# Performance work log

Hardware: AMD Instinct MI355X
Metric: run time of the kernel (lower is better)

## Reference

```python
import jax, jax.numpy as jnp
import numpy as np

SEQ_LEN = 48
OUT_DIM = 3
EMB_DIM = 32
HID_DIM = 96
BATCH = 131072


def setup_inputs() -> dict:
    key = jax.random.key(0)
    ks = jax.random.split(key, 12)
    s_emb = 1.0 / np.sqrt(OUT_DIM)
    s_gru = 1.0 / np.sqrt(HID_DIM)
    s_out = 1.0 / np.sqrt(HID_DIM)
    u = lambda k, shp, s: jax.random.uniform(k, shp, jnp.float32, -s, s)
    return {
        "last_pos_rel": jax.random.normal(ks[0], (BATCH, OUT_DIM), jnp.float32),
        "past_encoded": jax.random.normal(ks[1], (1, BATCH, HID_DIM // 2), jnp.float32),
        "future_encoded": jax.random.normal(ks[2], (1, BATCH, HID_DIM // 2), jnp.float32),
        "W_emb": u(ks[3], (EMB_DIM, OUT_DIM), s_emb),
        "b_emb": u(ks[4], (EMB_DIM,), s_emb),
        "W_ih": u(ks[5], (3 * HID_DIM, EMB_DIM), s_gru),
        "W_hh": u(ks[6], (3 * HID_DIM, HID_DIM), s_gru),
        "b_ih": u(ks[7], (3 * HID_DIM,), s_gru),
        "b_hh": u(ks[8], (3 * HID_DIM,), s_gru),
        "W_out": u(ks[9], (OUT_DIM, HID_DIM), s_out),
        "b_out": u(ks[10], (OUT_DIM,), s_out),
    }


def reference(last_pos_rel, past_encoded, future_encoded, W_emb, b_emb,
              W_ih, W_hh, b_ih, b_hh, W_out, b_out):
    # initial hidden state: concat of the two 48-dim encodings -> (B, 96)
    h0 = jnp.concatenate([past_encoded, future_encoded], axis=2)[0]
    # initial decoder input: spatial embedding of last relative position
    x0 = last_pos_rel @ W_emb.T + b_emb  # (B, EMB)

    def step(carry, _):
        h, x = carry
        gx = x @ W_ih.T + b_ih   # (B, 3H)
        gh = h @ W_hh.T + b_hh   # (B, 3H)
        gxr, gxz, gxn = jnp.split(gx, 3, axis=-1)
        ghr, ghz, ghn = jnp.split(gh, 3, axis=-1)
        r = jax.nn.sigmoid(gxr + ghr)
        z = jax.nn.sigmoid(gxz + ghz)
        n = jnp.tanh(gxn + r * ghn)
        h_new = (1.0 - z) * n + z * h
        rel_pos = h_new @ W_out.T + b_out       # (B, 3)
        x_new = rel_pos @ W_emb.T + b_emb       # (B, EMB)
        return (h_new, x_new), rel_pos

    _, pred_traj = jax.lax.scan(step, (h0, x0), None, length=SEQ_LEN)
    return pred_traj  # (SEQ_LEN, B, 3)
```

## Files before the change

### kernel.cpp

```cpp
#include <hip/hip_runtime.h>
#include <hip/hip_bf16.h>
#include <type_traits>

#define SEQ_LEN 48
#define HID     96
#define NB      131072
#define MROWS   304
#define ABYTES  (MROWS*HID*2)
#define COEF_OFF_F (ABYTES/4)
#define COEF_FLOATS (96*16)
#define BOUT_OFF_F (COEF_OFF_F + COEF_FLOATS)
#define LDS_U4  ((ABYTES + COEF_FLOATS*4)/16)

typedef __attribute__((ext_vector_type(4))) float f32x4;
typedef __attribute__((ext_vector_type(8))) __bf16 bf16x8;
typedef unsigned int uint;
typedef unsigned short ushort;

__device__ __forceinline__ float sigm(float x) {
    return __builtin_amdgcn_rcpf(1.f + __expf(-x));
}
__device__ __forceinline__ float tanh_(float y) {
    return 1.f - 2.f * __builtin_amdgcn_rcpf(__expf(2.f * y) + 1.f);
}
__device__ __forceinline__ uint packbf(float a, float b) {
    ushort lo = __builtin_bit_cast(ushort, __float2bfloat16(a));
    ushort hi = __builtin_bit_cast(ushort, __float2bfloat16(b));
    return (uint)lo | ((uint)hi << 16);
}

__global__ void fold_k(const float* __restrict__ W_emb, const float* __restrict__ b_emb,
                       const float* __restrict__ W_ih,  const float* __restrict__ W_hh,
                       const float* __restrict__ b_ih,  const float* __restrict__ b_hh,
                       const float* __restrict__ W_out, const float* __restrict__ b_out,
                       void* wsv)
{
    ushort* A  = (ushort*)wsv;
    float*  CF = (float*)wsv + COEF_OFF_F;
    float*  BO = (float*)wsv + BOUT_OFF_F;
    int g = blockIdx.x * 64 + threadIdx.x;
    if (g < 3) BO[g] = b_out[g];

    auto wxe_row = [&](int gg, float* w, float& bx) {
        w[0] = w[1] = w[2] = 0.f; bx = b_ih[gg];
        for (int e = 0; e < 32; e++) {
            float wi = W_ih[gg * 32 + e];
            w[0] += wi * W_emb[e * 3 + 0];
            w[1] += wi * W_emb[e * 3 + 1];
            w[2] += wi * W_emb[e * 3 + 2];
            bx   += wi * b_emb[e];
        }
    };

    if (g < MROWS) {
        float w[3] = {0.f, 0.f, 0.f}, bx = 0.f;
        if (g < 192) wxe_row(g, w, bx);
        for (int k = 0; k < HID; k++) {
            float val;
            if      (g < 192) val = W_hh[g * HID + k] + w[0]*W_out[0*HID+k] + w[1]*W_out[1*HID+k] + w[2]*W_out[2*HID+k];
            else if (g < 288) val = W_hh[g * HID + k];
            else if (g < 291) val = W_out[(g - 288) * HID + k];
            else              val = 0.f;
            int t = g >> 4, c = k >> 5, l = (g & 15) | (((k >> 3) & 3) << 4), i = k & 7;
            A[((t * 3 + c) * 64 + l) * 8 + i] = __builtin_bit_cast(ushort, __float2bfloat16(val));
        }
    }
    if (g < 96) {
        int j = g;
        float wn[3], bxn; wxe_row(192 + j, wn, bxn);
        float wr[3], bxr; wxe_row(j,        wr, bxr);
        float wz[3], bxz; wxe_row(96 + j,   wz, bxz);
        float quads[4][4] = {
            { wn[0], wn[1], wn[2], bxn },
            { b_hh[192 + j],
              bxr + b_hh[j]      + wr[0]*b_out[0] + wr[1]*b_out[1] + wr[2]*b_out[2],
              bxz + b_hh[96 + j] + wz[0]*b_out[0] + wz[1]*b_out[1] + wz[2]*b_out[2],
              0.f },
            { wr[0], wr[1], wr[2], wz[0] },
            { wz[1], wz[2], 0.f, 0.f }
        };
        int qj = (j >> 2) & 3;
        float* row = CF + j * 16;
        for (int L = 0; L < 4; ++L) {
            int p = (L + qj) & 3;
            row[p * 4 + 0] = quads[L][0];
            row[p * 4 + 1] = quads[L][1];
            row[p * 4 + 2] = quads[L][2];
            row[p * 4 + 3] = quads[L][3];
        }
    }
}

__global__ __launch_bounds__(256, 2)
void gru_mfma(const float* __restrict__ last_pos, const float* __restrict__ past,
              const float* __restrict__ fut, const void* __restrict__ wsv,
              float* __restrict__ out)
{
    __shared__ uint4 sb[LDS_U4];
    const int tid = threadIdx.x;
    const uint4* gsrc = (const uint4*)wsv;
    #pragma unroll
    for (int it = 0; it < 16; ++it) { int idx = tid + it * 256; if (idx < LDS_U4) sb[idx] = gsrc[idx]; }
    __syncthreads();

    const float* CF  = (const float*)sb + COEF_OFF_F;
    const float* BOg = (const float*)wsv + BOUT_OFF_F;
    const float bo[3] = {BOg[0], BOg[1], BOg[2]};

    const int lane = tid & 63;
    const int wid  = tid >> 6;
    const int b    = lane & 15;
    const int q    = lane >> 4;
    const int row0 = blockIdx.x * 64 + wid * 16 + b;

    uint hpk[6][2];
    #pragma unroll
    for (int t = 0; t < 6; ++t) {
        const float* src = (t < 3) ? (past + (size_t)row0 * 48 + t * 16 + q * 4)
                                   : (fut  + (size_t)row0 * 48 + (t - 3) * 16 + q * 4);
        f32x4 v = *(const f32x4*)src;
        hpk[t][0] = packbf(v[0], v[1]);
        hpk[t][1] = packbf(v[2], v[3]);
    }

    const int idxA = 4 * (b | ((((q << 1) + 0) & 3) << 4));
    const int idxB = 4 * (b | ((((q << 1) + 1) & 3) << 4));
    uint4 bfu[3];
    auto do_exchange = [&]() {
        #pragma unroll
        for (int c = 0; c < 3; ++c)
            #pragma unroll
            for (int dd = 0; dd < 4; ++dd) {
                int idx = (dd < 2) ? idxA : idxB;
                int va = __builtin_amdgcn_ds_bpermute(idx, (int)hpk[2 * c][dd & 1]);
                int vb = __builtin_amdgcn_ds_bpermute(idx, (int)hpk[2 * c + 1][dd & 1]);
                bfu[c][dd] = (uint)((lane < 32) ? va : vb);
            }
    };
    do_exchange();

    float pc[3];
    pc[0] = last_pos[(size_t)row0 * 3 + 0];
    pc[1] = last_pos[(size_t)row0 * 3 + 1];
    pc[2] = last_pos[(size_t)row0 * 3 + 2];

    const f32x4 zero4 = {0.f, 0.f, 0.f, 0.f};
    const int p0r = (0 + q) & 3, p1r = (1 + q) & 3, p2r = (2 + q) & 3, p3r = (3 + q) & 3;

    auto tile18 = [&]() -> f32x4 {
        f32x4 a18;
        #pragma unroll
        for (int c = 0; c < 3; ++c) {
            bf16x8 a = __builtin_bit_cast(bf16x8, sb[(18 * 3 + c) * 64 + lane]);
            bf16x8 bb = __builtin_bit_cast(bf16x8, bfu[c]);
            a18 = __builtin_amdgcn_mfma_f32_16x16x32_bf16(a, bb, (c == 0) ? zero4 : a18, 0, 0, 0);
        }
        return a18;
    };

    auto do_groups = [&](auto FIRST_c, const float* d0) {
        constexpr bool FIRST = decltype(FIRST_c)::value;
        #pragma unroll
        for (int t = 0; t < 6; ++t) {
            f32x4 aR, aZ, aN;
            #pragma unroll
            for (int c = 0; c < 3; ++c) {
                bf16x8 fr = __builtin_bit_cast(bf16x8, sb[((t)      * 3 + c) * 64 + lane]);
                bf16x8 fz = __builtin_bit_cast(bf16x8, sb[((6 + t)  * 3 + c) * 64 + lane]);
                bf16x8 fn = __builtin_bit_cast(bf16x8, sb[((12 + t) * 3 + c) * 64 + lane]);
                bf16x8 bb = __builtin_bit_cast(bf16x8, bfu[c]);
                aR = __builtin_amdgcn_mfma_f32_16x16x32_bf16(fr, bb, (c == 0) ? zero4 : aR, 0, 0, 0);
                aZ = __builtin_amdgcn_mfma_f32_16x16x32_bf16(fz, bb, (c == 0) ? zero4 : aZ, 0, 0, 0);
                aN = __builtin_amdgcn_mfma_f32_16x16x32_bf16(fn, bb, (c == 0) ? zero4 : aN, 0, 0, 0);
            }
            const float* cbase = CF + (16 * t + 4 * q) * 16;
            uint np0 = 0, np1 = 0;
            #pragma unroll
            for (int r = 0; r < 4; ++r) {
                f32x4 ca = *(const f32x4*)(cbase + 16 * r + 4 * p0r);
                f32x4 cb = *(const f32x4*)(cbase + 16 * r + 4 * p1r);
                float sr  = aR[r] + cb[1];
                float sz  = aZ[r] + cb[2];
                float ghn = aN[r] + cb[0];
                float gxn = ca[3] + pc[0]*ca[0] + pc[1]*ca[1] + pc[2]*ca[2];
                if constexpr (FIRST) {
                    f32x4 c2 = *(const f32x4*)(cbase + 16 * r + 4 * p2r);
                    f32x4 c3 = *(const f32x4*)(cbase + 16 * r + 4 * p3r);
                    sr += d0[0]*c2[0] + d0[1]*c2[1] + d0[2]*c2[2];
                    sz += d0[0]*c2[3] + d0[1]*c3[0] + d0[2]*c3[1];
                }
                float rg = sigm(sr);
                float zg = sigm(sz);
                float ng = tanh_(gxn + rg * ghn);
                uint pk = hpk[t][r >> 1];
                float hold = __builtin_bit_cast(float, (r & 1) ? (pk & 0xffff0000u) : (pk << 16));
                float hv = ng + zg * (hold - ng);
                ushort hb = __builtin_bit_cast(ushort, __float2bfloat16(hv));
                if      (r == 0) np0 = hb;
                else if (r == 1) np0 |= (uint)hb << 16;
                else if (r == 2) np1 = hb;
                else             np1 |= (uint)hb << 16;
            }
            hpk[t][0] = np0;
            hpk[t][1] = np1;
            __builtin_amdgcn_sched_barrier(0);
        }
    };

    {
        f32x4 a18 = tile18();
        float d0[3];
        #pragma unroll
        for (int o = 0; o < 3; ++o) {
            float po = a18[o] + bo[o];
            float pb = __builtin_bit_cast(float,
                        __builtin_amdgcn_ds_bpermute(4 * b, __builtin_bit_cast(int, po)));
            d0[o] = pc[o] - pb;
        }
        __builtin_amdgcn_sched_barrier(0);
        do_groups(std::integral_constant<bool, true>{}, d0);
        do_exchange();
    }

    #pragma unroll 1
    for (int s = 1; s < SEQ_LEN; ++s) {
        f32x4 a18 = tile18();
        #pragma unroll
        for (int o = 0; o < 3; ++o) {
            float po = a18[o] + bo[o];
            float pb = __builtin_bit_cast(float,
                        __builtin_amdgcn_ds_bpermute(4 * b, __builtin_bit_cast(int, po)));
            if (q == 0) out[((size_t)(s - 1) * NB + row0) * 3 + o] = po;
            pc[o] = pb;
        }
        __builtin_amdgcn_sched_barrier(0);
        do_groups(std::integral_constant<bool, false>{}, nullptr);
        do_exchange();
    }

    {
        f32x4 f18 = tile18();
        if (q == 0) {
            #pragma unroll
            for (int o = 0; o < 3; ++o)
                out[((size_t)47 * NB + row0) * 3 + o] = f18[o] + bo[o];
        }
    }
}

extern "C" void kernel_launch(void* const* d_in, const int* in_sizes, int n_in,
                              void* d_out, int out_size, void* d_ws, size_t ws_size,
                              hipStream_t stream)
{
    const float* last_pos = (const float*)d_in[0];
    const float* past     = (const float*)d_in[1];
    const float* fut      = (const float*)d_in[2];
    const float* W_emb    = (const float*)d_in[3];
    const float* b_emb    = (const float*)d_in[4];
    const float* W_ih     = (const float*)d_in[5];
    const float* W_hh     = (const float*)d_in[6];
    const float* b_ih     = (const float*)d_in[7];
    const float* b_hh     = (const float*)d_in[8];
    const float* W_out    = (const float*)d_in[9];
    const float* b_out    = (const float*)d_in[10];
    float* out = (float*)d_out;

    hipLaunchKernelGGL(fold_k, dim3(5), dim3(64), 0, stream,
                       W_emb, b_emb, W_ih, W_hh, b_ih, b_hh, W_out, b_out, d_ws);
    hipLaunchKernelGGL(gru_mfma, dim3(NB / 64), dim3(256), 0, stream,
                       last_pos, past, fut, d_ws, out);
}
```

Before: 842.7 us.

## Fold log2(e) into GRU weights and use 512-thread blocks

The preprocessing kernel now pre-scales the r/z gate weights and biases by log2(e) and the n-gate terms by 2*log2(e). The recurrent kernel can then call the hardware exp2 directly, dropping one multiply per transcendental in the inner gate math. Separately, blocks grow to 512 threads covering 128 rows, with launch bounds asking for 4 blocks per CU. That tightens the per-thread register budget, which may force spills, and the roughly 64 KB of LDS per block likely caps real residency below the requested 4 blocks.

```diff
diff --git a/kernel.cpp b/kernel.cpp
--- a/kernel.cpp
+++ b/kernel.cpp
@@ -17,11 +17,11 @@
 typedef unsigned int uint;
 typedef unsigned short ushort;
 
-__device__ __forceinline__ float sigm(float x) {
-    return __builtin_amdgcn_rcpf(1.f + __expf(-x));
-}
-__device__ __forceinline__ float tanh_(float y) {
-    return 1.f - 2.f * __builtin_amdgcn_rcpf(__expf(2.f * y) + 1.f);
+__device__ __forceinline__ float sigm2(float xp) {
+    return __builtin_amdgcn_rcpf(1.f + __builtin_amdgcn_exp2f(-xp));
+}
+__device__ __forceinline__ float tanh2(float yp) {
+    return 1.f - 2.f * __builtin_amdgcn_rcpf(__builtin_amdgcn_exp2f(yp) + 1.f);
 }
 __device__ __forceinline__ uint packbf(float a, float b) {
     ushort lo = __builtin_bit_cast(ushort, __float2bfloat16(a));
@@ -35,6 +35,8 @@
                        const float* __restrict__ W_out, const float* __restrict__ b_out,
                        void* wsv)
 {
+    const float L2E  = 1.44269504088896340736f;
+    const float L2E2 = 2.f * L2E;
     ushort* A  = (ushort*)wsv;
     float*  CF = (float*)wsv + COEF_OFF_F;
     float*  BO = (float*)wsv + BOUT_OFF_F;
@@ -57,8 +59,8 @@
         if (g < 192) wxe_row(g, w, bx);
         for (int k = 0; k < HID; k++) {
             float val;
-            if      (g < 192) val = W_hh[g * HID + k] + w[0]*W_out[0*HID+k] + w[1]*W_out[1*HID+k] + w[2]*W_out[2*HID+k];
-            else if (g < 288) val = W_hh[g * HID + k];
+            if      (g < 192) val = (W_hh[g * HID + k] + w[0]*W_out[0*HID+k] + w[1]*W_out[1*HID+k] + w[2]*W_out[2*HID+k]) * L2E;
+            else if (g < 288) val = W_hh[g * HID + k] * L2E2;
             else if (g < 291) val = W_out[(g - 288) * HID + k];
             else              val = 0.f;
             int t = g >> 4, c = k >> 5, l = (g & 15) | (((k >> 3) & 3) << 4), i = k & 7;
@@ -71,13 +73,13 @@
         float wr[3], bxr; wxe_row(j,        wr, bxr);
         float wz[3], bxz; wxe_row(96 + j,   wz, bxz);
         float quads[4][4] = {
-            { wn[0], wn[1], wn[2], bxn },
-            { b_hh[192 + j],
-              bxr + b_hh[j]      + wr[0]*b_out[0] + wr[1]*b_out[1] + wr[2]*b_out[2],
-              bxz + b_hh[96 + j] + wz[0]*b_out[0] + wz[1]*b_out[1] + wz[2]*b_out[2],
+            { wn[0]*L2E2, wn[1]*L2E2, wn[2]*L2E2, bxn*L2E2 },
+            { b_hh[192 + j]*L2E2,
+              (bxr + b_hh[j]      + wr[0]*b_out[0] + wr[1]*b_out[1] + wr[2]*b_out[2]) * L2E,
+              (bxz + b_hh[96 + j] + wz[0]*b_out[0] + wz[1]*b_out[1] + wz[2]*b_out[2]) * L2E,
               0.f },
-            { wr[0], wr[1], wr[2], wz[0] },
-            { wz[1], wz[2], 0.f, 0.f }
+            { wr[0]*L2E, wr[1]*L2E, wr[2]*L2E, wz[0]*L2E },
+            { wz[1]*L2E, wz[2]*L2E, 0.f, 0.f }
         };
         int qj = (j >> 2) & 3;
         float* row = CF + j * 16;
@@ -91,7 +93,7 @@
     }
 }
 
-__global__ __launch_bounds__(256, 2)
+__global__ __launch_bounds__(512, 4)
 void gru_mfma(const float* __restrict__ last_pos, const float* __restrict__ past,
               const float* __restrict__ fut, const void* __restrict__ wsv,
               float* __restrict__ out)
@@ -100,7 +102,7 @@
     const int tid = threadIdx.x;
     const uint4* gsrc = (const uint4*)wsv;
     #pragma unroll
-    for (int it = 0; it < 16; ++it) { int idx = tid + it * 256; if (idx < LDS_U4) sb[idx] = gsrc[idx]; }
+    for (int it = 0; it < 8; ++it) { int idx = tid + it * 512; if (idx < LDS_U4) sb[idx] = gsrc[idx]; }
     __syncthreads();
 
     const float* CF  = (const float*)sb + COEF_OFF_F;
@@ -111,7 +113,7 @@
     const int wid  = tid >> 6;
     const int b    = lane & 15;
     const int q    = lane >> 4;
-    const int row0 = blockIdx.x * 64 + wid * 16 + b;
+    const int row0 = blockIdx.x * 128 + wid * 16 + b;
 
     uint hpk[6][2];
     #pragma unroll
@@ -189,9 +191,9 @@
                     sr += d0[0]*c2[0] + d0[1]*c2[1] + d0[2]*c2[2];
                     sz += d0[0]*c2[3] + d0[1]*c3[0] + d0[2]*c3[1];
                 }
-                float rg = sigm(sr);
-                float zg = sigm(sz);
-                float ng = tanh_(gxn + rg * ghn);
+                float rg = sigm2(sr);
+                float zg = sigm2(sz);
+                float ng = tanh2(gxn + rg * ghn);
                 uint pk = hpk[t][r >> 1];
                 float hold = __builtin_bit_cast(float, (r & 1) ? (pk & 0xffff0000u) : (pk << 16));
                 float hv = ng + zg * (hold - ng);
@@ -267,6 +269,6 @@
 
     hipLaunchKernelGGL(fold_k, dim3(5), dim3(64), 0, stream,
                        W_emb, b_emb, W_ih, W_hh, b_ih, b_hh, W_out, b_out, d_ws);
-    hipLaunchKernelGGL(gru_mfma, dim3(NB / 64), dim3(256), 0, stream,
+    hipLaunchKernelGGL(gru_mfma, dim3(NB / 128), dim3(512), 0, stream,
                        last_pos, past, fut, d_ws, out);
 }
```

Measured after the change: 871.2 us. 3.4% more time.
